# Optimization experiments

Measured on AMD Instinct MI355X. Metric: run time of the kernel, lower is better.

The kernel has to match this reference:

```python
import jax, jax.numpy as jnp
import numpy as np

S, B, H = 2048, 32, 1024

def setup_inputs() -> dict:
    key = jax.random.key(0)
    ks = jax.random.split(key, 8)
    return {
        "hidden": jax.random.normal(ks[0], (1, B, H), dtype=jnp.float32),
        "hidden_sequence": jax.random.normal(ks[1], (S, B, H), dtype=jnp.float32),
        "input_masks": jax.random.bernoulli(ks[2], 0.5, (S, B)),
        "W1": jax.random.normal(ks[3], (H, H), dtype=jnp.float32) * 0.02,
        "b1": jax.random.normal(ks[4], (H,), dtype=jnp.float32) * 0.02,
        "W2": jax.random.normal(ks[5], (H, H), dtype=jnp.float32) * 0.02,
        "b2": jax.random.normal(ks[6], (H,), dtype=jnp.float32) * 0.02,
        "v": jax.random.uniform(ks[7], (H,), dtype=jnp.float32),
    }

def reference(hidden, hidden_sequence, input_masks, W1, b1, W2, b2, v):
    # hidden: (1,B,H) broadcast over S; hidden_sequence: (S,B,H)
    # additive (Bahdanau) energy: v . tanh(W1 hs + W2 h)  -> (S,B)
    pre = (jnp.einsum('sbh,kh->sbk', hidden_sequence, W1) + b1
           + jnp.einsum('obh,kh->obk', hidden, W2) + b2)  # (S,B,H)
    energy = jnp.einsum('sbh,h->sb', jnp.tanh(pre), v)     # (S,B)
    energy = jnp.where(input_masks, energy, jnp.float32(-1e10))
    attn = jax.nn.softmax(energy, axis=0)                  # softmax over seq per batch
    context = jnp.einsum('sb,sbh->bh', attn, hidden_sequence)[None]  # (1,B,H)
    return context
```

## Files before the change

### kernel.cpp

```cpp
#include <hip/hip_runtime.h>
#include <stdint.h>


#define SS 2048
#define BB 32
#define HH 1024
#define MM (SS*BB)

typedef _Float16 f16;
typedef __attribute__((ext_vector_type(8))) _Float16 f16x8;
typedef __attribute__((ext_vector_type(4))) _Float16 f16x4;
typedef __attribute__((ext_vector_type(4))) float   floatx4;

__device__ __forceinline__ float tanh_fast(float x) {
  float e = __expf(2.0f * x);
  return 1.0f - 2.0f / (e + 1.0f);
}

__device__ __forceinline__ void gload16(void* lds_base, const void* gptr) {
  __builtin_amdgcn_global_load_lds(
      (const __attribute__((address_space(1))) uint32_t*)(uintptr_t)gptr,
      (__attribute__((address_space(3))) uint32_t*)(uint32_t)(uintptr_t)lds_base,
      16, 0, 0);
}

#define BAR()   __builtin_amdgcn_s_barrier()
#define VMC4()  asm volatile("s_waitcnt vmcnt(4)" ::: "memory")
#define VMC0()  asm volatile("s_waitcnt vmcnt(0)" ::: "memory")

__device__ __forceinline__ float dpp_red16(float x) {
  int t;
  t = __builtin_amdgcn_update_dpp(0, __float_as_int(x), 0xB1, 0xF, 0xF, true);
  x += __int_as_float(t);
  t = __builtin_amdgcn_update_dpp(0, __float_as_int(x), 0x4E, 0xF, 0xF, true);
  x += __int_as_float(t);
  t = __builtin_amdgcn_update_dpp(0, __float_as_int(x), 0x141, 0xF, 0xF, true);
  x += __int_as_float(t);
  t = __builtin_amdgcn_update_dpp(0, __float_as_int(x), 0x140, 0xF, 0xF, true);
  x += __int_as_float(t);
  return x;
}

__global__ __launch_bounds__(256) void prep_kernel(
    const float* __restrict__ hs, const float* __restrict__ W1,
    const float* __restrict__ hidden, const float* __restrict__ W2,
    const float* __restrict__ b1, const float* __restrict__ b2,
    f16* __restrict__ hsf, f16* __restrict__ W1f, float* __restrict__ t2)
{
  const int bid = blockIdx.x;
  if (bid < 33280) {
    const size_t NH = (size_t)MM * HH;
    size_t g0 = (size_t)bid * 2048 + threadIdx.x * 4;
    const float* src;
    f16* dst;
    if (g0 < NH) { src = hs; dst = hsf; }
    else         { src = W1 - NH; dst = W1f - NH; }
    floatx4 a = *(const floatx4*)&src[g0];
    floatx4 b = *(const floatx4*)&src[g0 + 1024];
    f16x4 oa = {(f16)a.x,(f16)a.y,(f16)a.z,(f16)a.w};
    f16x4 ob = {(f16)b.x,(f16)b.y,(f16)b.z,(f16)b.w};
    *(f16x4*)&dst[g0] = oa;
    *(f16x4*)&dst[g0 + 1024] = ob;
  } else {
    const int gw   = (bid - 33280) * 4 + (threadIdx.x >> 6);
    const int n    = gw >> 5;
    const int b    = gw & 31;
    const int lane = threadIdx.x & 63;
    float acc = 0.f;
#pragma unroll
    for (int q = 0; q < 4; ++q) {
      floatx4 hv = *(const floatx4*)&hidden[b * HH + q * 256 + lane * 4];
      floatx4 wv = *(const floatx4*)&W2[(size_t)n * HH + q * 256 + lane * 4];
      acc += hv.x * wv.x + hv.y * wv.y + hv.z * wv.z + hv.w * wv.w;
    }
#pragma unroll
    for (int off = 1; off < 64; off <<= 1) acc += __shfl_xor(acc, off);
    if (lane == 0) t2[b * HH + n] = acc + b1[n] + b2[n];
  }
}

__global__ __launch_bounds__(512, 2) void gemm_energy_8p(
    const f16* __restrict__ hsf, const f16* __restrict__ W1f,
    const float* __restrict__ t2, const float* __restrict__ v,
    float* __restrict__ epart)
{
  __shared__ __align__(16) f16 Asm[2][2][128 * 64];
  __shared__ __align__(16) f16 Bsm[2][2][128 * 64];

  const int tid  = threadIdx.x;
  const int lane = tid & 63;
  const int w    = tid >> 6;
  const int quad = lane >> 4;
  const int l15  = lane & 15;
  const int wr   = w >> 2;
  const int wc   = w & 3;

  const int l  = blockIdx.x;
  const int x  = l & 7;
  const int j_ = l >> 3;
  const int nb = j_ & 3;
  const int mt = (j_ >> 2) * 8 + x;
  const int mB = mt * 256;
  const int nB = nb * 256;

  const int srow = w * 8 + (lane >> 3);
  const int sc0  = lane & 7;

  auto stA = [&](int buf, int half, int kt) {
#pragma unroll
    for (int q = 0; q < 2; ++q) {
      const int r  = q * 64 + srow;
      const int cb = sc0 ^ (r & 7);
      gload16(&Asm[buf][half][(q * 64 + w * 8) * 64],
              &hsf[(size_t)(mB + half * 128 + r) * HH + kt + cb * 8]);
    }
  };
  auto stB = [&](int buf, int half, int kt) {
#pragma unroll
    for (int q = 0; q < 2; ++q) {
      const int r  = q * 64 + srow;
      const int cb = sc0 ^ (r & 7);
      gload16(&Bsm[buf][half][(q * 64 + w * 8) * 64],
              &W1f[(size_t)(nB + half * 128 + r) * HH + kt + cb * 8]);
    }
  };

  floatx4 acc[8][4];
#pragma unroll
  for (int i = 0; i < 8; ++i)
#pragma unroll
    for (int j = 0; j < 4; ++j) acc[i][j] = (floatx4){0.f, 0.f, 0.f, 0.f};

  stB(0, 0, 0); stA(0, 0, 0); stA(0, 1, 0); stB(0, 1, 0);
  stB(1, 0, 64); stA(1, 0, 64);
  VMC4();
  BAR();

  f16x8 aF[2][4], b0F[2][2], b1F[2][2];
  const int bhalf  = wc >> 1;
  const int brbase = (wc & 1) * 64;

#pragma unroll 2
  for (int t = 0; t < 16; ++t) {
    const int buf = t & 1, nbuf = buf ^ 1;
    const int kt1 = (t + 1) * 64, kt2 = (t + 2) * 64;

#pragma unroll
    for (int ks = 0; ks < 2; ++ks) {
#pragma unroll
      for (int i = 0; i < 4; ++i) {
        const int rl = i * 16 + l15;
        const int cb = (ks * 4 + quad) ^ (rl & 7);
        aF[ks][i] = *(const f16x8*)&Asm[buf][wr][(rl * 8 + cb) * 8];
      }
#pragma unroll
      for (int j = 0; j < 2; ++j) {
        const int rl = brbase + j * 16 + l15;
        const int cb = (ks * 4 + quad) ^ (rl & 7);
        b0F[ks][j] = *(const f16x8*)&Bsm[buf][bhalf][(rl * 8 + cb) * 8];
      }
    }
    if (t < 15) stA(nbuf, 1, kt1);
    __builtin_amdgcn_s_setprio(1);
#pragma unroll
    for (int ks = 0; ks < 2; ++ks)
#pragma unroll
      for (int i = 0; i < 4; ++i)
#pragma unroll
        for (int j = 0; j < 2; ++j)
          acc[i][j] = __builtin_amdgcn_mfma_f32_16x16x32_f16(aF[ks][i], b0F[ks][j], acc[i][j], 0, 0, 0);
    __builtin_amdgcn_s_setprio(0);
    BAR();

#pragma unroll
    for (int ks = 0; ks < 2; ++ks)
#pragma unroll
      for (int j = 0; j < 2; ++j) {
        const int rl = brbase + (j + 2) * 16 + l15;
        const int cb = (ks * 4 + quad) ^ (rl & 7);
        b1F[ks][j] = *(const f16x8*)&Bsm[buf][bhalf][(rl * 8 + cb) * 8];
      }
    if (t < 15) stB(nbuf, 1, kt1);
    __builtin_amdgcn_s_setprio(1);
#pragma unroll
    for (int ks = 0; ks < 2; ++ks)
#pragma unroll
      for (int i = 0; i < 4; ++i)
#pragma unroll
        for (int j = 0; j < 2; ++j)
          acc[i][2 + j] = __builtin_amdgcn_mfma_f32_16x16x32_f16(aF[ks][i], b1F[ks][j], acc[i][2 + j], 0, 0, 0);
    __builtin_amdgcn_s_setprio(0);
    BAR();

#pragma unroll
    for (int ks = 0; ks < 2; ++ks)
#pragma unroll
      for (int i = 0; i < 4; ++i) {
        const int rl = 64 + i * 16 + l15;
        const int cb = (ks * 4 + quad) ^ (rl & 7);
        aF[ks][i] = *(const f16x8*)&Asm[buf][wr][(rl * 8 + cb) * 8];
      }
    if (t < 14) stB(buf, 0, kt2);
    __builtin_amdgcn_s_setprio(1);
#pragma unroll
    for (int ks = 0; ks < 2; ++ks)
#pragma unroll
      for (int i = 0; i < 4; ++i)
#pragma unroll
        for (int j = 0; j < 2; ++j)
          acc[4 + i][2 + j] = __builtin_amdgcn_mfma_f32_16x16x32_f16(aF[ks][i], b1F[ks][j], acc[4 + i][2 + j], 0, 0, 0);
    __builtin_amdgcn_s_setprio(0);
    BAR();

    if (t < 14) stA(buf, 0, kt2);
    __builtin_amdgcn_s_setprio(1);
#pragma unroll
    for (int ks = 0; ks < 2; ++ks)
#pragma unroll
      for (int i = 0; i < 4; ++i)
#pragma unroll
        for (int j = 0; j < 2; ++j)
          acc[4 + i][j] = __builtin_amdgcn_mfma_f32_16x16x32_f16(aF[ks][i], b0F[ks][j], acc[4 + i][j], 0, 0, 0);
    __builtin_amdgcn_s_setprio(0);
    if (t < 14) { VMC4(); } else { VMC0(); }
    BAR();
  }

  float* t2s = (float*)&Asm[0][0][0];
  {
    const int r = tid >> 4;
    const int c = (tid & 15) * 16;
#pragma unroll
    for (int q = 0; q < 4; ++q) {
      floatx4 tv = *(const floatx4*)&t2[r * HH + nB + c + q * 4];
      *(floatx4*)&t2s[r * 257 + c + q * 4] = tv;
    }
  }
  __syncthreads();

  float vv[4];
#pragma unroll
  for (int j = 0; j < 4; ++j) vv[j] = v[nB + wc * 64 + j * 16 + l15];
#pragma unroll
  for (int i = 0; i < 8; ++i) {
#pragma unroll
    for (int reg = 0; reg < 4; ++reg) {
      const int m = mB + wr * 128 + i * 16 + quad * 4 + reg;
      const int b = m & (BB - 1);
      const int s = m >> 5;
      float rs = 0.f;
#pragma unroll
      for (int j = 0; j < 4; ++j) {
        const int n = wc * 64 + j * 16 + l15;
        rs += tanh_fast(acc[i][j][reg] + t2s[b * 257 + n]) * vv[j];
      }
      rs = dpp_red16(rs);
      if (l15 == 0) epart[(size_t)(nb * 4 + wc) * MM + b * SS + s] = rs;
    }
  }
}

__global__ __launch_bounds__(1024) void softmax16t(
    const float* __restrict__ epart, const int* __restrict__ masks,
    float* __restrict__ attn)
{
  const int b = blockIdx.x;
  const int tid = threadIdx.x;
  __shared__ float redm[16], reds[16];
  float em[2];
  float lmax = -3e38f;
#pragma unroll
  for (int it = 0; it < 2; ++it) {
    const int s = it * 1024 + tid;
    float e = 0.f;
#pragma unroll
    for (int p = 0; p < 16; ++p) e += epart[(size_t)p * MM + b * SS + s];
    if (masks[s * BB + b] == 0) e = -1e10f;
    em[it] = e;
    lmax = fmaxf(lmax, e);
  }
#pragma unroll
  for (int off = 1; off < 64; off <<= 1) lmax = fmaxf(lmax, __shfl_xor(lmax, off));
  if ((tid & 63) == 0) redm[tid >> 6] = lmax;
  __syncthreads();
#pragma unroll
  for (int i = 0; i < 16; ++i) lmax = fmaxf(lmax, redm[i]);
  float lsum = 0.f;
#pragma unroll
  for (int it = 0; it < 2; ++it) { em[it] = __expf(em[it] - lmax); lsum += em[it]; }
#pragma unroll
  for (int off = 1; off < 64; off <<= 1) lsum += __shfl_xor(lsum, off);
  if ((tid & 63) == 0) reds[tid >> 6] = lsum;
  __syncthreads();
  float tsum = 0.f;
#pragma unroll
  for (int i = 0; i < 16; ++i) tsum += reds[i];
  const float inv = 1.0f / tsum;
#pragma unroll
  for (int it = 0; it < 2; ++it) attn[b * SS + it * 1024 + tid] = em[it] * inv;
}

__global__ __launch_bounds__(256) void context_f16t(
    const f16* __restrict__ hsf, const float* __restrict__ attn,
    float* __restrict__ ctxp)
{
  const int b  = blockIdx.x;
  const int sc = blockIdx.y;
  const int tid = threadIdx.x;
  __shared__ float sat[64];
  if (tid < 64) sat[tid] = attn[b * SS + sc * 64 + tid];
  __syncthreads();
  floatx4 acc = {0.f, 0.f, 0.f, 0.f};
#pragma unroll 4
  for (int s = 0; s < 64; ++s) {
    const float a = sat[s];
    if (a != 0.f) {
      f16x4 h = *(const f16x4*)&hsf[(size_t)((sc * 64 + s) * BB + b) * HH + tid * 4];
      acc.x += a * (float)h[0];
      acc.y += a * (float)h[1];
      acc.z += a * (float)h[2];
      acc.w += a * (float)h[3];
    }
  }
  *(floatx4*)&ctxp[(size_t)(sc * BB + b) * HH + tid * 4] = acc;
}

__global__ __launch_bounds__(256) void ctx_reduce32(
    const float* __restrict__ ctxp, float* __restrict__ out)
{
  const int i = blockIdx.x * 256 + threadIdx.x;
  float s = 0.f;
#pragma unroll
  for (int sc = 0; sc < 32; ++sc) s += ctxp[(size_t)sc * (BB * HH) + i];
  out[i] = s;
}

__global__ __launch_bounds__(256) void t2_kernel(
    const float* __restrict__ hidden, const float* __restrict__ W2,
    const float* __restrict__ b1, const float* __restrict__ b2,
    float* __restrict__ t2)
{
  const int gw   = blockIdx.x * 4 + (threadIdx.x >> 6);
  const int n    = gw >> 5;
  const int b    = gw & 31;
  const int lane = threadIdx.x & 63;
  float acc = 0.f;
#pragma unroll
  for (int q = 0; q < 4; ++q) {
    floatx4 hv = *(const floatx4*)&hidden[b * HH + q * 256 + lane * 4];
    floatx4 wv = *(const floatx4*)&W2[(size_t)n * HH + q * 256 + lane * 4];
    acc += hv.x * wv.x + hv.y * wv.y + hv.z * wv.z + hv.w * wv.w;
  }
#pragma unroll
  for (int off = 1; off < 64; off <<= 1) acc += __shfl_xor(acc, off);
  if (lane == 0) t2[b * HH + n] = acc + b1[n] + b2[n];
}

__global__ __launch_bounds__(256) void gemm_energy_fb(
    const float* __restrict__ hs, const float* __restrict__ W1,
    const float* __restrict__ t2, const float* __restrict__ v,
    float* __restrict__ epart)
{
  const int tid = threadIdx.x;
  const int nb  = blockIdx.x;
  const int mB  = blockIdx.y * 128;
  __shared__ __align__(16) f16 Asm[128][72];
  __shared__ __align__(16) f16 Bsm[128][72];
  const int lane = tid & 63;
  const int w    = tid >> 6;
  const int quad = lane >> 4;
  const int l15  = lane & 15;
  floatx4 acc[2][8];
#pragma unroll
  for (int i = 0; i < 2; ++i)
#pragma unroll
    for (int j = 0; j < 8; ++j) acc[i][j] = (floatx4){0.f, 0.f, 0.f, 0.f};
  const int srow = tid >> 4;
  const int scol = (tid & 15) * 4;
  const float* Abase = hs + (size_t)(mB + srow) * HH + scol;
  const float* Bbase = W1 + (size_t)(nb * 128 + srow) * HH + scol;
  for (int kt = 0; kt < HH; kt += 64) {
#pragma unroll
    for (int p = 0; p < 8; ++p) {
      floatx4 fa = *(const floatx4*)(Abase + (size_t)(p * 16) * HH + kt);
      floatx4 fb = *(const floatx4*)(Bbase + (size_t)(p * 16) * HH + kt);
      f16x4 ha = {(f16)fa.x, (f16)fa.y, (f16)fa.z, (f16)fa.w};
      f16x4 hb = {(f16)fb.x, (f16)fb.y, (f16)fb.z, (f16)fb.w};
      *(f16x4*)&Asm[p * 16 + srow][scol] = ha;
      *(f16x4*)&Bsm[p * 16 + srow][scol] = hb;
    }
    __syncthreads();
#pragma unroll
    for (int ks = 0; ks < 2; ++ks) {
      f16x8 af[2], bfr[8];
#pragma unroll
      for (int i = 0; i < 2; ++i)
        af[i] = *(const f16x8*)&Asm[w * 32 + i * 16 + l15][ks * 32 + quad * 8];
#pragma unroll
      for (int j = 0; j < 8; ++j)
        bfr[j] = *(const f16x8*)&Bsm[j * 16 + l15][ks * 32 + quad * 8];
#pragma unroll
      for (int i = 0; i < 2; ++i)
#pragma unroll
        for (int j = 0; j < 8; ++j)
          acc[i][j] = __builtin_amdgcn_mfma_f32_16x16x32_f16(af[i], bfr[j], acc[i][j], 0, 0, 0);
    }
    __syncthreads();
  }
  const int nB = nb * 128;
#pragma unroll
  for (int i = 0; i < 2; ++i) {
#pragma unroll
    for (int reg = 0; reg < 4; ++reg) {
      const int m = mB + w * 32 + i * 16 + quad * 4 + reg;
      const int b = m & (BB - 1);
      float rs = 0.f;
#pragma unroll
      for (int j = 0; j < 8; ++j) {
        const int n = nB + j * 16 + l15;
        rs += tanh_fast(acc[i][j][reg] + t2[b * HH + n]) * v[n];
      }
      rs += __shfl_xor(rs, 1);
      rs += __shfl_xor(rs, 2);
      rs += __shfl_xor(rs, 4);
      rs += __shfl_xor(rs, 8);
      if (l15 == 0) epart[(size_t)nb * MM + m] = rs;
    }
  }
}

__global__ __launch_bounds__(256) void softmax8(
    const float* __restrict__ epart, const int* __restrict__ masks,
    float* __restrict__ attn)
{
  const int b = blockIdx.x;
  const int tid = threadIdx.x;
  __shared__ float redm[4], reds[4];
  float em[8];
  float lmax = -3e38f;
#pragma unroll
  for (int it = 0; it < 8; ++it) {
    const int s = it * 256 + tid;
    float e = 0.f;
#pragma unroll
    for (int p = 0; p < 8; ++p) e += epart[(size_t)p * MM + s * BB + b];
    if (masks[s * BB + b] == 0) e = -1e10f;
    em[it] = e;
    lmax = fmaxf(lmax, e);
  }
#pragma unroll
  for (int off = 1; off < 64; off <<= 1) lmax = fmaxf(lmax, __shfl_xor(lmax, off));
  if ((tid & 63) == 0) redm[tid >> 6] = lmax;
  __syncthreads();
  lmax = fmaxf(fmaxf(redm[0], redm[1]), fmaxf(redm[2], redm[3]));
  float lsum = 0.f;
#pragma unroll
  for (int it = 0; it < 8; ++it) { em[it] = __expf(em[it] - lmax); lsum += em[it]; }
#pragma unroll
  for (int off = 1; off < 64; off <<= 1) lsum += __shfl_xor(lsum, off);
  if ((tid & 63) == 0) reds[tid >> 6] = lsum;
  __syncthreads();
  const float inv = 1.0f / (reds[0] + reds[1] + reds[2] + reds[3]);
#pragma unroll
  for (int it = 0; it < 8; ++it) attn[(it * 256 + tid) * BB + b] = em[it] * inv;
}

__global__ __launch_bounds__(256) void context_fb(
    const float* __restrict__ hs, const float* __restrict__ attn,
    float* __restrict__ ctxp)
{
  const int b  = blockIdx.x;
  const int sc = blockIdx.y;
  const int tid = threadIdx.x;
  floatx4 acc = {0.f, 0.f, 0.f, 0.f};
  for (int s = sc * 256; s < sc * 256 + 256; ++s) {
    const float a = attn[s * BB + b];
    if (a != 0.f) {
      floatx4 h = *(const floatx4*)&hs[(size_t)(s * BB + b) * HH + tid * 4];
      acc.x += a * h.x; acc.y += a * h.y; acc.z += a * h.z; acc.w += a * h.w;
    }
  }
  *(floatx4*)&ctxp[(size_t)(sc * BB + b) * HH + tid * 4] = acc;
}

__global__ __launch_bounds__(256) void ctx_reduce8(
    const float* __restrict__ ctxp, float* __restrict__ out)
{
  const int i = blockIdx.x * 256 + threadIdx.x;
  float s = 0.f;
#pragma unroll
  for (int sc = 0; sc < 8; ++sc) s += ctxp[(size_t)sc * (BB * HH) + i];
  out[i] = s;
}

extern "C" void kernel_launch(void* const* d_in, const int* in_sizes, int n_in,
                              void* d_out, int out_size, void* d_ws, size_t ws_size,
                              hipStream_t stream) {
  const float* hidden = (const float*)d_in[0];
  const float* hs     = (const float*)d_in[1];
  const int*   masks  = (const int*)d_in[2];
  const float* W1     = (const float*)d_in[3];
  const float* b1     = (const float*)d_in[4];
  const float* W2     = (const float*)d_in[5];
  const float* b2     = (const float*)d_in[6];
  const float* v      = (const float*)d_in[7];
  float* out = (float*)d_out;

  const size_t hsf_b   = (size_t)MM * HH * 2;
  const size_t w1f_b   = (size_t)HH * HH * 2;
  const size_t epart_b = (size_t)16 * MM * 4;
  const size_t attn_b  = (size_t)MM * 4;
  const size_t t2_b    = (size_t)BB * HH * 4;
  const size_t ctxp_b  = (size_t)32 * BB * HH * 4;
  const size_t need = hsf_b + w1f_b + epart_b + attn_b + t2_b + ctxp_b;

  if (ws_size >= need) {
    char* p = (char*)d_ws;
    f16*   hsf   = (f16*)p;              p += hsf_b;
    f16*   W1f   = (f16*)p;              p += w1f_b;
    float* epart = (float*)p;            p += epart_b;
    float* attn  = (float*)p;            p += attn_b;
    float* t2    = (float*)p;            p += t2_b;
    float* ctxp  = (float*)p;

    prep_kernel<<<dim3(33280 + 8192), 256, 0, stream>>>(hs, W1, hidden, W2, b1, b2, hsf, W1f, t2);
    gemm_energy_8p<<<dim3(1024), 512, 0, stream>>>(hsf, W1f, t2, v, epart);
    softmax16t<<<dim3(BB), 1024, 0, stream>>>(epart, masks, attn);
    context_f16t<<<dim3(BB, 32), 256, 0, stream>>>(hsf, attn, ctxp);
    ctx_reduce32<<<dim3(BB * HH / 256), 256, 0, stream>>>(ctxp, out);
  } else {
    float* epart = (float*)d_ws;
    float* attn  = epart + 8 * MM;
    float* t2    = attn + MM;
    float* ctxp  = t2 + BB * HH;

    t2_kernel<<<dim3(BB * HH / 4), 256, 0, stream>>>(hidden, W2, b1, b2, t2);
    gemm_energy_fb<<<dim3(8, MM / 128), 256, 0, stream>>>(hs, W1, t2, v, epart);
    softmax8<<<dim3(BB), 256, 0, stream>>>(epart, masks, attn);
    context_fb<<<dim3(BB, 8), 256, 0, stream>>>(hs, attn, ctxp);
    ctx_reduce8<<<dim3(BB * HH / 256), 256, 0, stream>>>(ctxp, out);
  }
}
```

Before: 569.5 us.

## Restructure GEMM main loop to defer hi-A quadrant MFMA across iterations

Reorganizes the double-buffered MFMA main loop so the A-high by B0 quadrant from the previous k-tile is computed at the start of the next iteration, using register-held fragments. It issues all next-tile A and B loads at the top of each iteration and waits for all loads with vmcnt(0) before the barrier, replacing the earlier staggered two-ahead prefetch with partial waits. Barriers become asm volatile with memory clobbers. The aim is to overlap LDS reads and global loads with MFMA work and simplify waits. In exchange it holds more fragment registers, which may hurt occupancy, and the full vmcnt(0) wait per iteration reduces prefetch depth.

```diff
diff --git a/kernel.cpp b/kernel.cpp
--- a/kernel.cpp
+++ b/kernel.cpp
@@ -24,8 +24,7 @@
       16, 0, 0);
 }
 
-#define BAR()   __builtin_amdgcn_s_barrier()
-#define VMC4()  asm volatile("s_waitcnt vmcnt(4)" ::: "memory")
+#define BARm()  asm volatile("s_barrier" ::: "memory")
 #define VMC0()  asm volatile("s_waitcnt vmcnt(0)" ::: "memory")
 
 __device__ __forceinline__ float dpp_red16(float x) {
@@ -131,36 +130,47 @@
 #pragma unroll
     for (int j = 0; j < 4; ++j) acc[i][j] = (floatx4){0.f, 0.f, 0.f, 0.f};
 
-  stB(0, 0, 0); stA(0, 0, 0); stA(0, 1, 0); stB(0, 1, 0);
-  stB(1, 0, 64); stA(1, 0, 64);
-  VMC4();
-  BAR();
-
-  f16x8 aF[2][4], b0F[2][2], b1F[2][2];
+  stA(0, 0, 0); stA(0, 1, 0); stB(0, 0, 0); stB(0, 1, 0);
+  VMC0();
+  BARm();
+
+  f16x8 aLo[2][4], aHi[2][4], b0F[2][2][2], b1F[2][2];
+  {
+    f16x8 z = {};
+#pragma unroll
+    for (int ks = 0; ks < 2; ++ks) {
+#pragma unroll
+      for (int i = 0; i < 4; ++i) aHi[ks][i] = z;
+#pragma unroll
+      for (int j = 0; j < 2; ++j) b0F[1][ks][j] = z;
+    }
+  }
+
   const int bhalf  = wc >> 1;
   const int brbase = (wc & 1) * 64;
 
 #pragma unroll 2
   for (int t = 0; t < 16; ++t) {
     const int buf = t & 1, nbuf = buf ^ 1;
-    const int kt1 = (t + 1) * 64, kt2 = (t + 2) * 64;
-
+    const int pp = buf, pq = nbuf;
+    const int kt1 = (t + 1) * 64;
+
+    if (t < 15) { stA(nbuf, 0, kt1); stA(nbuf, 1, kt1); }
 #pragma unroll
     for (int ks = 0; ks < 2; ++ks) {
 #pragma unroll
       for (int i = 0; i < 4; ++i) {
         const int rl = i * 16 + l15;
         const int cb = (ks * 4 + quad) ^ (rl & 7);
-        aF[ks][i] = *(const f16x8*)&Asm[buf][wr][(rl * 8 + cb) * 8];
+        aLo[ks][i] = *(const f16x8*)&Asm[buf][wr][(rl * 8 + cb) * 8];
       }
 #pragma unroll
       for (int j = 0; j < 2; ++j) {
         const int rl = brbase + j * 16 + l15;
         const int cb = (ks * 4 + quad) ^ (rl & 7);
-        b0F[ks][j] = *(const f16x8*)&Bsm[buf][bhalf][(rl * 8 + cb) * 8];
+        b0F[pp][ks][j] = *(const f16x8*)&Bsm[buf][bhalf][(rl * 8 + cb) * 8];
       }
     }
-    if (t < 15) stA(nbuf, 1, kt1);
     __builtin_amdgcn_s_setprio(1);
 #pragma unroll
     for (int ks = 0; ks < 2; ++ks)
@@ -168,10 +178,11 @@
       for (int i = 0; i < 4; ++i)
 #pragma unroll
         for (int j = 0; j < 2; ++j)
-          acc[i][j] = __builtin_amdgcn_mfma_f32_16x16x32_f16(aF[ks][i], b0F[ks][j], acc[i][j], 0, 0, 0);
+          acc[4 + i][j] = __builtin_amdgcn_mfma_f32_16x16x32_f16(aHi[ks][i], b0F[pq][ks][j], acc[4 + i][j], 0, 0, 0);
     __builtin_amdgcn_s_setprio(0);
-    BAR();
-
+    BARm();
+
+    if (t < 15) { stB(nbuf, 0, kt1); stB(nbuf, 1, kt1); }
 #pragma unroll
     for (int ks = 0; ks < 2; ++ks)
 #pragma unroll
@@ -180,7 +191,6 @@
         const int cb = (ks * 4 + quad) ^ (rl & 7);
         b1F[ks][j] = *(const f16x8*)&Bsm[buf][bhalf][(rl * 8 + cb) * 8];
       }
-    if (t < 15) stB(nbuf, 1, kt1);
     __builtin_amdgcn_s_setprio(1);
 #pragma unroll
     for (int ks = 0; ks < 2; ++ks)
@@ -188,9 +198,9 @@
       for (int i = 0; i < 4; ++i)
 #pragma unroll
         for (int j = 0; j < 2; ++j)
-          acc[i][2 + j] = __builtin_amdgcn_mfma_f32_16x16x32_f16(aF[ks][i], b1F[ks][j], acc[i][2 + j], 0, 0, 0);
+          acc[i][j] = __builtin_amdgcn_mfma_f32_16x16x32_f16(aLo[ks][i], b0F[pp][ks][j], acc[i][j], 0, 0, 0);
     __builtin_amdgcn_s_setprio(0);
-    BAR();
+    BARm();
 
 #pragma unroll
     for (int ks = 0; ks < 2; ++ks)
@@ -198,9 +208,8 @@
       for (int i = 0; i < 4; ++i) {
         const int rl = 64 + i * 16 + l15;
         const int cb = (ks * 4 + quad) ^ (rl & 7);
-        aF[ks][i] = *(const f16x8*)&Asm[buf][wr][(rl * 8 + cb) * 8];
+        aHi[ks][i] = *(const f16x8*)&Asm[buf][wr][(rl * 8 + cb) * 8];
       }
-    if (t < 14) stB(buf, 0, kt2);
     __builtin_amdgcn_s_setprio(1);
 #pragma unroll
     for (int ks = 0; ks < 2; ++ks)
@@ -208,11 +217,10 @@
       for (int i = 0; i < 4; ++i)
 #pragma unroll
         for (int j = 0; j < 2; ++j)
-          acc[4 + i][2 + j] = __builtin_amdgcn_mfma_f32_16x16x32_f16(aF[ks][i], b1F[ks][j], acc[4 + i][2 + j], 0, 0, 0);
+          acc[i][2 + j] = __builtin_amdgcn_mfma_f32_16x16x32_f16(aLo[ks][i], b1F[ks][j], acc[i][2 + j], 0, 0, 0);
     __builtin_amdgcn_s_setprio(0);
-    BAR();
-
-    if (t < 14) stA(buf, 0, kt2);
+    BARm();
+
     __builtin_amdgcn_s_setprio(1);
 #pragma unroll
     for (int ks = 0; ks < 2; ++ks)
@@ -220,11 +228,21 @@
       for (int i = 0; i < 4; ++i)
 #pragma unroll
         for (int j = 0; j < 2; ++j)
-          acc[4 + i][j] = __builtin_amdgcn_mfma_f32_16x16x32_f16(aF[ks][i], b0F[ks][j], acc[4 + i][j], 0, 0, 0);
+          acc[4 + i][2 + j] = __builtin_amdgcn_mfma_f32_16x16x32_f16(aHi[ks][i], b1F[ks][j], acc[4 + i][2 + j], 0, 0, 0);
     __builtin_amdgcn_s_setprio(0);
-    if (t < 14) { VMC4(); } else { VMC0(); }
-    BAR();
-  }
+    VMC0();
+    BARm();
+  }
+
+  __builtin_amdgcn_s_setprio(1);
+#pragma unroll
+  for (int ks = 0; ks < 2; ++ks)
+#pragma unroll
+    for (int i = 0; i < 4; ++i)
+#pragma unroll
+      for (int j = 0; j < 2; ++j)
+        acc[4 + i][j] = __builtin_amdgcn_mfma_f32_16x16x32_f16(aHi[ks][i], b0F[1][ks][j], acc[4 + i][j], 0, 0, 0);
+  __builtin_amdgcn_s_setprio(0);
 
   float* t2s = (float*)&Asm[0][0][0];
   {
```

Measured after the change: 624.4 us. 1.1x slower.

## Split softmax into partial-chunk stats and fold normalization into context kernel

Applied to the files above, without the earlier changes.

Replaces the single-block-per-batch softmax (32 blocks of 1024 threads) with 256 blocks that each compute a chunk max and sum-of-exp. The context kernel merges the chunk stats and normalizes the attention weights itself, so the separate normalized attn pass disappears. The context split is also reduced from 32 to 8 sequence chunks per batch, which shrinks the partial buffer and the final reduction but leaves only 256 context blocks, each running a longer serial loop.

```diff
diff --git a/kernel.cpp b/kernel.cpp
--- a/kernel.cpp
+++ b/kernel.cpp
@@ -260,62 +260,68 @@
   }
 }
 
-__global__ __launch_bounds__(1024) void softmax16t(
+__global__ __launch_bounds__(256) void smax_part(
     const float* __restrict__ epart, const int* __restrict__ masks,
-    float* __restrict__ attn)
-{
-  const int b = blockIdx.x;
+    float* __restrict__ e_buf, float* __restrict__ stats)
+{
+  const int b   = blockIdx.x >> 3;
+  const int c   = blockIdx.x & 7;
   const int tid = threadIdx.x;
-  __shared__ float redm[16], reds[16];
-  float em[2];
-  float lmax = -3e38f;
-#pragma unroll
-  for (int it = 0; it < 2; ++it) {
-    const int s = it * 1024 + tid;
-    float e = 0.f;
-#pragma unroll
-    for (int p = 0; p < 16; ++p) e += epart[(size_t)p * MM + b * SS + s];
-    if (masks[s * BB + b] == 0) e = -1e10f;
-    em[it] = e;
-    lmax = fmaxf(lmax, e);
-  }
-#pragma unroll
-  for (int off = 1; off < 64; off <<= 1) lmax = fmaxf(lmax, __shfl_xor(lmax, off));
-  if ((tid & 63) == 0) redm[tid >> 6] = lmax;
+  const int s   = c * 256 + tid;
+  __shared__ float redm[4], reds[4];
+
+  float e = 0.f;
+#pragma unroll
+  for (int p = 0; p < 16; ++p) e += epart[(size_t)p * MM + b * SS + s];
+  if (masks[s * BB + b] == 0) e = -1e10f;
+  e_buf[b * SS + s] = e;
+
+  float m = e;
+#pragma unroll
+  for (int off = 1; off < 64; off <<= 1) m = fmaxf(m, __shfl_xor(m, off));
+  if ((tid & 63) == 0) redm[tid >> 6] = m;
   __syncthreads();
-#pragma unroll
-  for (int i = 0; i < 16; ++i) lmax = fmaxf(lmax, redm[i]);
-  float lsum = 0.f;
-#pragma unroll
-  for (int it = 0; it < 2; ++it) { em[it] = __expf(em[it] - lmax); lsum += em[it]; }
-#pragma unroll
-  for (int off = 1; off < 64; off <<= 1) lsum += __shfl_xor(lsum, off);
-  if ((tid & 63) == 0) reds[tid >> 6] = lsum;
+  m = fmaxf(fmaxf(redm[0], redm[1]), fmaxf(redm[2], redm[3]));
+
+  float x = __expf(e - m);
+#pragma unroll
+  for (int off = 1; off < 64; off <<= 1) x += __shfl_xor(x, off);
+  if ((tid & 63) == 0) reds[tid >> 6] = x;
   __syncthreads();
-  float tsum = 0.f;
-#pragma unroll
-  for (int i = 0; i < 16; ++i) tsum += reds[i];
-  const float inv = 1.0f / tsum;
-#pragma unroll
-  for (int it = 0; it < 2; ++it) attn[b * SS + it * 1024 + tid] = em[it] * inv;
-}
-
-__global__ __launch_bounds__(256) void context_f16t(
-    const f16* __restrict__ hsf, const float* __restrict__ attn,
-    float* __restrict__ ctxp)
-{
-  const int b  = blockIdx.x;
-  const int sc = blockIdx.y;
+  if (tid == 0) {
+    const float sum = reds[0] + reds[1] + reds[2] + reds[3];
+    stats[(b * 8 + c) * 2 + 0] = m;
+    stats[(b * 8 + c) * 2 + 1] = sum;
+  }
+}
+
+__global__ __launch_bounds__(256) void context8(
+    const f16* __restrict__ hsf, const float* __restrict__ e_buf,
+    const float* __restrict__ stats, float* __restrict__ ctxp)
+{
+  const int b   = blockIdx.x;
+  const int sc  = blockIdx.y;
   const int tid = threadIdx.x;
-  __shared__ float sat[64];
-  if (tid < 64) sat[tid] = attn[b * SS + sc * 64 + tid];
+
+  float gmax = -3e38f;
+#pragma unroll
+  for (int c = 0; c < 8; ++c) gmax = fmaxf(gmax, stats[(b * 8 + c) * 2]);
+  float gsum = 0.f;
+#pragma unroll
+  for (int c = 0; c < 8; ++c)
+    gsum += stats[(b * 8 + c) * 2 + 1] * __expf(stats[(b * 8 + c) * 2] - gmax);
+  const float inv = 1.0f / gsum;
+
+  __shared__ float sat[256];
+  sat[tid] = __expf(e_buf[b * SS + sc * 256 + tid] - gmax) * inv;
   __syncthreads();
+
   floatx4 acc = {0.f, 0.f, 0.f, 0.f};
 #pragma unroll 4
-  for (int s = 0; s < 64; ++s) {
+  for (int s = 0; s < 256; ++s) {
     const float a = sat[s];
     if (a != 0.f) {
-      f16x4 h = *(const f16x4*)&hsf[(size_t)((sc * 64 + s) * BB + b) * HH + tid * 4];
+      f16x4 h = *(const f16x4*)&hsf[(size_t)((sc * 256 + s) * BB + b) * HH + tid * 4];
       acc.x += a * (float)h[0];
       acc.y += a * (float)h[1];
       acc.z += a * (float)h[2];
@@ -325,13 +331,13 @@
   *(floatx4*)&ctxp[(size_t)(sc * BB + b) * HH + tid * 4] = acc;
 }
 
-__global__ __launch_bounds__(256) void ctx_reduce32(
+__global__ __launch_bounds__(256) void ctx_reduce8(
     const float* __restrict__ ctxp, float* __restrict__ out)
 {
   const int i = blockIdx.x * 256 + threadIdx.x;
   float s = 0.f;
 #pragma unroll
-  for (int sc = 0; sc < 32; ++sc) s += ctxp[(size_t)sc * (BB * HH) + i];
+  for (int sc = 0; sc < 8; ++sc) s += ctxp[(size_t)sc * (BB * HH) + i];
   out[i] = s;
 }
 
@@ -481,16 +487,6 @@
     }
   }
   *(floatx4*)&ctxp[(size_t)(sc * BB + b) * HH + tid * 4] = acc;
-}
-
-__global__ __launch_bounds__(256) void ctx_reduce8(
-    const float* __restrict__ ctxp, float* __restrict__ out)
-{
-  const int i = blockIdx.x * 256 + threadIdx.x;
-  float s = 0.f;
-#pragma unroll
-  for (int sc = 0; sc < 8; ++sc) s += ctxp[(size_t)sc * (BB * HH) + i];
-  out[i] = s;
 }
 
 extern "C" void kernel_launch(void* const* d_in, const int* in_sizes, int n_in,
@@ -509,25 +505,27 @@
   const size_t hsf_b   = (size_t)MM * HH * 2;
   const size_t w1f_b   = (size_t)HH * HH * 2;
   const size_t epart_b = (size_t)16 * MM * 4;
-  const size_t attn_b  = (size_t)MM * 4;
+  const size_t ebuf_b  = (size_t)MM * 4;
+  const size_t stats_b = (size_t)4096;
   const size_t t2_b    = (size_t)BB * HH * 4;
-  const size_t ctxp_b  = (size_t)32 * BB * HH * 4;
-  const size_t need = hsf_b + w1f_b + epart_b + attn_b + t2_b + ctxp_b;
+  const size_t ctxp_b  = (size_t)8 * BB * HH * 4;
+  const size_t need = hsf_b + w1f_b + epart_b + ebuf_b + stats_b + t2_b + ctxp_b;
 
   if (ws_size >= need) {
     char* p = (char*)d_ws;
     f16*   hsf   = (f16*)p;              p += hsf_b;
     f16*   W1f   = (f16*)p;              p += w1f_b;
     float* epart = (float*)p;            p += epart_b;
-    float* attn  = (float*)p;            p += attn_b;
+    float* e_buf = (float*)p;            p += ebuf_b;
+    float* stats = (float*)p;            p += stats_b;
     float* t2    = (float*)p;            p += t2_b;
     float* ctxp  = (float*)p;
 
     prep_kernel<<<dim3(33280 + 8192), 256, 0, stream>>>(hs, W1, hidden, W2, b1, b2, hsf, W1f, t2);
     gemm_energy_8p<<<dim3(1024), 512, 0, stream>>>(hsf, W1f, t2, v, epart);
-    softmax16t<<<dim3(BB), 1024, 0, stream>>>(epart, masks, attn);
-    context_f16t<<<dim3(BB, 32), 256, 0, stream>>>(hsf, attn, ctxp);
-    ctx_reduce32<<<dim3(BB * HH / 256), 256, 0, stream>>>(ctxp, out);
+    smax_part<<<dim3(256), 256, 0, stream>>>(epart, masks, e_buf, stats);
+    context8<<<dim3(BB, 8), 256, 0, stream>>>(hsf, e_buf, stats, ctxp);
+    ctx_reduce8<<<dim3(BB * HH / 256), 256, 0, stream>>>(ctxp, out);
   } else {
     float* epart = (float*)d_ws;
     float* attn  = epart + 8 * MM;
```

Measured after the change: 588.1 us. 1.03x slower.
